# Kernel tuning notes

Hardware: AMD Instinct MI355X
Metric: run time of the kernel (lower is better)

The kernel has to match this reference:

```python
import jax, jax.numpy as jnp
import numpy as np

EPS = 1e-12


def setup_inputs() -> dict:
    key = jax.random.key(0)
    k1, k2, k3, k4, k5, k6 = jax.random.split(key, 6)
    N, R, T, D, depth = 50000, 1000, 400000, 256, 2
    features = jax.random.normal(k1, (N, D), dtype=jnp.float32)
    rel_emb = jax.random.normal(k2, (R, D), dtype=jnp.float32)
    # xavier-style scale for [D,1] kernels, stored as [depth, D]
    attn_kernels = jax.random.normal(k3, (depth, D), dtype=jnp.float32) * np.sqrt(2.0 / (D + 1))
    r_val = jnp.ones((T,), dtype=jnp.float32)
    adj = jax.random.randint(k4, (2, T), 0, N, dtype=jnp.int64)
    r_index_tri = jnp.arange(T, dtype=jnp.int64)  # one relation per triple
    r_index_rel = jax.random.randint(k5, (T,), 0, R, dtype=jnp.int64)
    return {
        "features": features,
        "rel_emb": rel_emb,
        "attn_kernels": attn_kernels,
        "r_val": r_val,
        "adj": adj,
        "r_index_tri": r_index_tri,
        "r_index_rel": r_index_rel,
    }


def reference(features, rel_emb, attn_kernels, r_val, adj, r_index_tri, r_index_rel):
    N, D = features.shape
    T = adj.shape[1]
    depth = attn_kernels.shape[0]
    dst, src = adj[0], adj[1]  # softmax/aggregate over dst rows, gather neighbors via src

    x = jnp.tanh(features)
    outputs = [x]
    for l in range(depth):
        # sparse [T,R] @ rel_emb -> per-triple relation embedding [T, D]
        tri_rel = jax.ops.segment_sum(r_val[:, None] * rel_emb[r_index_rel], r_index_tri, num_segments=T)
        # L2 normalize per edge (torch F.normalize, eps=1e-12)
        norm = jnp.sqrt(jnp.sum(tri_rel * tri_rel, axis=1, keepdims=True))
        tri_rel = tri_rel / jnp.maximum(norm, EPS)
        # gather neighbor features and reflect across relation hyperplane
        neighs = x[src]  # [T, D]
        neighs = neighs - 2.0 * jnp.sum(neighs * tri_rel, axis=1, keepdims=True) * tri_rel
        # per-edge attention logits, segment softmax over destination rows
        att = tri_rel @ attn_kernels[l]  # [T]
        seg_max = jax.ops.segment_max(att, dst, num_segments=N)  # [N]
        e = jnp.exp(att - seg_max[dst])
        seg_sum = jax.ops.segment_sum(e, dst, num_segments=N)
        w = e / seg_sum[dst]  # [T]
        # scatter-sum weighted neighbor messages
        new_features = jax.ops.segment_sum(neighs * w[:, None], dst, num_segments=N)
        x = jnp.tanh(new_features)
        outputs.append(x)
    return jnp.concatenate(outputs, axis=-1)  # [N, D*(depth+1)]
```

## Files before the change

### kernel.cpp

```cpp
#include <hip/hip_runtime.h>
#include <hip/hip_bf16.h>
#include <hip/hip_fp16.h>

static constexpr int kN = 50000;
static constexpr int kR = 1000;
static constexpr int kT = 400000;
static constexpr int kD = 256;
static constexpr int kOutD = 768;
static constexpr int kNB = (kN + 255) / 256;

static constexpr size_t kOffRel16 = 2219008;
static constexpr size_t kOffXb0   = 2752512;
static constexpr size_t kXbBytes  = (size_t)kN * kD * 2;
static constexpr size_t kOffXb1   = kOffXb0 + kXbBytes;
static constexpr size_t kWsFull   = kOffXb1 + kXbBytes;
static constexpr int kShRowC = 1536;
static constexpr int kShOffC = 1024;

#define EPS_NORM 1e-12f

__device__ __forceinline__ float bf2f(__hip_bfloat16 h) { return __bfloat162float(h); }

__device__ __forceinline__ float4 h4f(ushort4 u) {
  float4 f;
  f.x = __half2float(__ushort_as_half(u.x));
  f.y = __half2float(__ushort_as_half(u.y));
  f.z = __half2float(__ushort_as_half(u.z));
  f.w = __half2float(__ushort_as_half(u.w));
  return f;
}

__device__ __forceinline__ float loadF(const void* p, int i, int f32m) {
  return f32m ? ((const float*)p)[i] : bf2f(((const __hip_bfloat16*)p)[i]);
}
__device__ __forceinline__ int loadI(const void* p, int i, int i64m) {
  return i64m ? (int)(((const long long*)p)[i]) : ((const int*)p)[i];
}

__global__ void __launch_bounds__(256) detect_kernel(
    const void* __restrict__ feat, const void* __restrict__ adj,
    int* __restrict__ flags) {
  __shared__ int s_f32, s_i64;
  if (threadIdx.x == 0) { s_f32 = 0; s_i64 = 1; }
  __syncthreads();
  const __hip_bfloat16* fb = (const __hip_bfloat16*)feat;
  for (int i = threadIdx.x; i < 4096; i += 256) {
    const float v = bf2f(fb[i]);
    if (!(fabsf(v) <= 64.f)) atomicExch(&s_f32, 1);
  }
  const int* ai = (const int*)adj;
  for (int i = threadIdx.x; i < 2048; i += 256) {
    if (ai[2 * i + 1] != 0) atomicExch(&s_i64, 0);
  }
  __syncthreads();
  if (threadIdx.x == 0) { flags[0] = s_f32; flags[1] = s_i64; }
}

__global__ void __launch_bounds__(256) relnorm_kernel(
    const void* __restrict__ rel_emb, const void* __restrict__ attn_k,
    __half* __restrict__ rel16, float* __restrict__ attL,
    const int* __restrict__ flags) {
  const int f32m = flags[0];
  const int r = blockIdx.x;
  const int d = threadIdx.x;
  const float v  = loadF(rel_emb, r * kD + d, f32m);
  const float k0 = loadF(attn_k, d, f32m);
  const float k1 = loadF(attn_k, kD + d, f32m);
  float ss = v * v, d0 = v * k0, d1 = v * k1;
#pragma unroll
  for (int off = 32; off > 0; off >>= 1) {
    ss += __shfl_xor(ss, off);
    d0 += __shfl_xor(d0, off);
    d1 += __shfl_xor(d1, off);
  }
  __shared__ float s_ss[4], s_d0[4], s_d1[4];
  const int wave = threadIdx.x >> 6, lane = threadIdx.x & 63;
  if (lane == 0) { s_ss[wave] = ss; s_d0[wave] = d0; s_d1[wave] = d1; }
  __syncthreads();
  const float tss = s_ss[0] + s_ss[1] + s_ss[2] + s_ss[3];
  const float inv = 1.0f / fmaxf(sqrtf(tss), EPS_NORM);
  rel16[r * kD + d] = __float2half(v * inv);
  if (threadIdx.x == 0) {
    attL[r]      = (s_d0[0] + s_d0[1] + s_d0[2] + s_d0[3]) * inv;
    attL[kR + r] = (s_d1[0] + s_d1[1] + s_d1[2] + s_d1[3]) * inv;
  }
}

__global__ void __launch_bounds__(256) x0_kernel(
    const void* __restrict__ feat, float* __restrict__ out,
    __half* __restrict__ xb, int xbRow, int xbOff,
    const int* __restrict__ flags) {
  const int f32m = flags[0];
  const int i4 = (blockIdx.x * 256 + threadIdx.x) * 4;
  float v0, v1, v2, v3;
  if (f32m) {
    const float4 f = ((const float4*)feat)[i4 >> 2];
    v0 = f.x; v1 = f.y; v2 = f.z; v3 = f.w;
  } else {
    union { ushort4 u; __hip_bfloat16 h[4]; } xu;
    xu.u = ((const ushort4*)feat)[i4 >> 2];
    v0 = bf2f(xu.h[0]); v1 = bf2f(xu.h[1]); v2 = bf2f(xu.h[2]); v3 = bf2f(xu.h[3]);
  }
  const int n = i4 >> 8, d = i4 & 255;
  float4 o; o.x = tanhf(v0); o.y = tanhf(v1); o.z = tanhf(v2); o.w = tanhf(v3);
  *(float4*)(out + (size_t)n * kOutD + d) = o;
  ushort4 h;
  h.x = __half_as_ushort(__float2half(o.x));
  h.y = __half_as_ushort(__float2half(o.y));
  h.z = __half_as_ushort(__float2half(o.z));
  h.w = __half_as_ushort(__float2half(o.w));
  *(ushort4*)(xb + (size_t)n * xbRow + xbOff + d) = h;
}

__global__ void __launch_bounds__(256) count_kernel(
    const void* __restrict__ adj, int* __restrict__ counts,
    const int* __restrict__ flags) {
  const int t = blockIdx.x * 256 + threadIdx.x;
  if (t >= kT) return;
  atomicAdd(&counts[loadI(adj, t, flags[1])], 1);
}

__global__ void __launch_bounds__(256) psum_kernel(
    const int* __restrict__ counts, int* __restrict__ partials) {
  const int i = blockIdx.x * 256 + threadIdx.x;
  int v = (i < kN) ? counts[i] : 0;
#pragma unroll
  for (int off = 32; off > 0; off >>= 1) v += __shfl_xor(v, off);
  __shared__ int sw[4];
  const int lane = threadIdx.x & 63, wv = threadIdx.x >> 6;
  if (lane == 0) sw[wv] = v;
  __syncthreads();
  if (threadIdx.x == 0) partials[blockIdx.x] = sw[0] + sw[1] + sw[2] + sw[3];
}

__global__ void __launch_bounds__(256) pscan_kernel(int* __restrict__ partials) {
  const int tid = threadIdx.x, lane = tid & 63, wv = tid >> 6;
  const int v = (tid < kNB) ? partials[tid] : 0;
  int x = v;
#pragma unroll
  for (int d = 1; d < 64; d <<= 1) {
    const int y = __shfl_up(x, d);
    if (lane >= d) x += y;
  }
  __shared__ int sw[4];
  if (lane == 63) sw[wv] = x;
  __syncthreads();
  int woff = 0;
  for (int w = 0; w < wv; ++w) woff += sw[w];
  if (tid < kNB) partials[tid] = woff + x - v;
}

__global__ void __launch_bounds__(256) offs_kernel(
    const int* __restrict__ counts, const int* __restrict__ partials,
    int* __restrict__ offsets, int* __restrict__ cursor) {
  const int i = blockIdx.x * 256 + threadIdx.x;
  const int lane = threadIdx.x & 63, wv = threadIdx.x >> 6;
  const int v = (i < kN) ? counts[i] : 0;
  int x = v;
#pragma unroll
  for (int d = 1; d < 64; d <<= 1) {
    const int y = __shfl_up(x, d);
    if (lane >= d) x += y;
  }
  __shared__ int sw[4];
  if (lane == 63) sw[wv] = x;
  __syncthreads();
  int woff = 0;
  for (int w = 0; w < wv; ++w) woff += sw[w];
  const int excl = partials[blockIdx.x] + woff + x - v;
  if (i < kN) { offsets[i] = excl; cursor[i] = excl; }
  if (i == 0) offsets[kN] = kT;
}

__global__ void __launch_bounds__(256) fill_kernel(
    const void* __restrict__ adj, int* __restrict__ cursor,
    int* __restrict__ perm, const int* __restrict__ flags) {
  const int t = blockIdx.x * 256 + threadIdx.x;
  if (t >= kT) return;
  const int d = loadI(adj, t, flags[1]);
  perm[atomicAdd(&cursor[d], 1)] = t;
}

template <int XF16>
__global__ void __launch_bounds__(256, 6) layer_kernel(
    const void* __restrict__ adj, const void* __restrict__ rrel,
    const void* __restrict__ r_val,
    const int* __restrict__ offsets, const int* __restrict__ perm,
    const float* __restrict__ xin,
    const __half* __restrict__ xbin, int xbRow, int xbOff,
    const __half* __restrict__ rel16, const float* __restrict__ attL_l,
    float* __restrict__ out, int col0,
    __half* __restrict__ xbout,
    const int* __restrict__ flags) {
  const int f32m = flags[0], i64m = flags[1];
  const int lane = threadIdx.x & 63;
  const int n = blockIdx.x * 4 + (threadIdx.x >> 6);
  const int beg = offsets[n];
  const int cnt = offsets[n + 1] - beg;
  float4 acc = make_float4(0.f, 0.f, 0.f, 0.f);
  float* orow = out + (size_t)n * kOutD + col0;

  if (cnt > 0 && cnt <= 64) {
    int pk_l = 0;
    float logit = -1e30f;
    if (lane < cnt) {
      const int t = perm[beg + lane];
      const float rv = loadF(r_val, t, f32m);
      const int r  = loadI(rrel, t, i64m);
      const int sn = loadI(adj, kT + t, i64m);
      const float sgn = (rv > 0.f) ? 1.f : ((rv < 0.f) ? -1.f : 0.f);
      logit = sgn * attL_l[r];
      pk_l = ((rv != 0.f ? 1 : 0) << 30) | (r << 17) | sn;
    }
    float m = logit;
    for (int off = 1; off < cnt; off <<= 1) m = fmaxf(m, __shfl_xor(m, off));
    const float e = (lane < cnt) ? __expf(logit - m) : 0.f;
    float s = e;
    for (int off = 1; off < cnt; off <<= 1) s += __shfl_xor(s, off);
    const float w_me = (lane < cnt) ? e / s : 0.f;

    for (int base = 0; base < cnt; base += 8) {
      int pk[8]; float wk[8];
#pragma unroll
      for (int k = 0; k < 8; ++k) {
        pk[k] = __shfl(pk_l, base + k);
        wk[k] = __shfl(w_me, base + k);
      }
      ushort4 ux[8], ur[8]; float4 xf[8];
#pragma unroll
      for (int k = 0; k < 8; ++k) {
        const int sn = pk[k] & 0x1FFFF;
        const int r  = (pk[k] >> 17) & 0x1FFF;
        if (XF16) ux[k] = *(const ushort4*)(xbin + (size_t)sn * xbRow + xbOff + lane * 4);
        else      xf[k] = *(const float4*)(xin + (size_t)sn * kOutD + lane * 4);
        ur[k] = *(const ushort4*)(rel16 + ((size_t)r << 8) + lane * 4);
      }
      float4 rn[8]; float dt[8];
#pragma unroll
      for (int k = 0; k < 8; ++k) {
        const float4 xv = XF16 ? h4f(ux[k]) : xf[k];
        rn[k] = h4f(ur[k]);
        dt[k] = xv.x * rn[k].x + xv.y * rn[k].y + xv.z * rn[k].z + xv.w * rn[k].w;
        acc.x += xv.x * wk[k]; acc.y += xv.y * wk[k];
        acc.z += xv.z * wk[k]; acc.w += xv.w * wk[k];
      }
#pragma unroll
      for (int off = 32; off > 0; off >>= 1) {
#pragma unroll
        for (int k = 0; k < 8; ++k) dt[k] += __shfl_xor(dt[k], off);
      }
#pragma unroll
      for (int k = 0; k < 8; ++k) {
        const float c = (((pk[k] >> 30) & 1) ? 2.f * wk[k] : 0.f) * dt[k];
        acc.x -= c * rn[k].x; acc.y -= c * rn[k].y;
        acc.z -= c * rn[k].z; acc.w -= c * rn[k].w;
      }
    }
  } else if (cnt > 64) {
    float lm = -1e30f;
    for (int i = lane; i < cnt; i += 64) {
      const int t = perm[beg + i];
      const float rv = loadF(r_val, t, f32m);
      const float sgn = (rv > 0.f) ? 1.f : ((rv < 0.f) ? -1.f : 0.f);
      lm = fmaxf(lm, sgn * attL_l[loadI(rrel, t, i64m)]);
    }
#pragma unroll
    for (int off = 32; off > 0; off >>= 1) lm = fmaxf(lm, __shfl_xor(lm, off));
    float ls = 0.f;
    for (int i = lane; i < cnt; i += 64) {
      const int t = perm[beg + i];
      const float rv = loadF(r_val, t, f32m);
      const float sgn = (rv > 0.f) ? 1.f : ((rv < 0.f) ? -1.f : 0.f);
      ls += __expf(sgn * attL_l[loadI(rrel, t, i64m)] - lm);
    }
#pragma unroll
    for (int off = 32; off > 0; off >>= 1) ls += __shfl_xor(ls, off);
    const float inv_s = 1.f / ls;

    for (int base = 0; base < cnt; base += 64) {
      const int nIn = min(64, cnt - base);
      int sn_l = 0, r_l = 0;
      float w_l = 0.f, s2_l = 0.f;
      if (lane < nIn) {
        const int t = perm[beg + base + lane];
        const float rv = loadF(r_val, t, f32m);
        r_l  = loadI(rrel, t, i64m);
        sn_l = loadI(adj, kT + t, i64m);
        const float sgn = (rv > 0.f) ? 1.f : ((rv < 0.f) ? -1.f : 0.f);
        w_l = __expf(sgn * attL_l[r_l] - lm) * inv_s;
        s2_l = (rv != 0.f) ? 1.f : 0.f;
      }
      for (int k = 0; k < nIn; ++k) {
        const int sn   = __shfl(sn_l, k);
        const int r    = __shfl(r_l, k);
        const float w  = __shfl(w_l, k);
        const float s2 = __shfl(s2_l, k);
        float4 xv;
        if (XF16) {
          xv = h4f(*(const ushort4*)(xbin + (size_t)sn * xbRow + xbOff + lane * 4));
        } else {
          xv = *(const float4*)(xin + (size_t)sn * kOutD + lane * 4);
        }
        const float4 rn = h4f(*(const ushort4*)(rel16 + ((size_t)r << 8) + lane * 4));
        float dot = xv.x * rn.x + xv.y * rn.y + xv.z * rn.z + xv.w * rn.w;
#pragma unroll
        for (int off = 32; off > 0; off >>= 1) dot += __shfl_xor(dot, off);
        const float c = 2.f * s2 * dot * w;
        acc.x += xv.x * w - c * rn.x;
        acc.y += xv.y * w - c * rn.y;
        acc.z += xv.z * w - c * rn.z;
        acc.w += xv.w * w - c * rn.w;
      }
    }
  }

  acc.x = tanhf(acc.x); acc.y = tanhf(acc.y);
  acc.z = tanhf(acc.z); acc.w = tanhf(acc.w);
  *(float4*)(orow + lane * 4) = acc;
  if (XF16 && xbout) {
    ushort4 h;
    h.x = __half_as_ushort(__float2half(acc.x));
    h.y = __half_as_ushort(__float2half(acc.y));
    h.z = __half_as_ushort(__float2half(acc.z));
    h.w = __half_as_ushort(__float2half(acc.w));
    *(ushort4*)(xbout + (size_t)n * kD + lane * 4) = h;
  }
}

extern "C" void kernel_launch(void* const* d_in, const int* in_sizes, int n_in,
                              void* d_out, int out_size, void* d_ws, size_t ws_size,
                              hipStream_t stream) {
  const void* features = d_in[0];
  const void* rel_emb  = d_in[1];
  const void* attn_k   = d_in[2];
  const void* r_val    = d_in[3];
  const void* adj      = d_in[4];
  const void* rrel     = d_in[6];
  float* out           = (float*)d_out;

  char* ws = (char*)d_ws;
  int*    flags    = (int*)(ws + 0);
  float*  attL     = (float*)(ws + 4096);
  int*    partials = (int*)(ws + 12288);
  int*    counts   = (int*)(ws + 16384);
  int*    offsets  = (int*)(ws + 217088);
  int*    cursor   = (int*)(ws + 417792);
  int*    perm     = (int*)(ws + 618496);
  __half* rel16    = (__half*)(ws + kOffRel16);
  const bool full = (ws_size >= kWsFull);
  __half* xb0 = full ? (__half*)(ws + kOffXb0) : (__half*)out;
  __half* xb1 = full ? (__half*)(ws + kOffXb1) : nullptr;
  const int xbRow0 = full ? kD : kShRowC;
  const int xbOff0 = full ? 0  : kShOffC;

  const int tb = (kT + 255) / 256;

  detect_kernel<<<1, 256, 0, stream>>>(features, adj, flags);
  relnorm_kernel<<<kR, 256, 0, stream>>>(rel_emb, attn_k, rel16, attL, flags);
  x0_kernel<<<kN * kD / 1024, 256, 0, stream>>>(features, out, xb0, xbRow0,
                                                xbOff0, flags);

  hipMemsetAsync(counts, 0, (size_t)kN * 4, stream);
  count_kernel<<<tb, 256, 0, stream>>>(adj, counts, flags);
  psum_kernel<<<kNB, 256, 0, stream>>>(counts, partials);
  pscan_kernel<<<1, 256, 0, stream>>>(partials);
  offs_kernel<<<kNB, 256, 0, stream>>>(counts, partials, offsets, cursor);
  fill_kernel<<<tb, 256, 0, stream>>>(adj, cursor, perm, flags);

  layer_kernel<1><<<kN / 4, 256, 0, stream>>>(adj, rrel, r_val, offsets, perm,
                                              nullptr, xb0, xbRow0, xbOff0,
                                              rel16, attL, out, kD, xb1, flags);
  if (full) {
    layer_kernel<1><<<kN / 4, 256, 0, stream>>>(adj, rrel, r_val, offsets, perm,
                                                nullptr, xb1, kD, 0,
                                                rel16, attL + kR, out, 2 * kD,
                                                nullptr, flags);
  } else {
    layer_kernel<0><<<kN / 4, 256, 0, stream>>>(adj, rrel, r_val, offsets, perm,
                                                out + kD, nullptr, 0, 0,
                                                rel16, attL + kR, out, 2 * kD,
                                                nullptr, flags);
  }
}
```

Measured before the change: 425.8 us.

## Pack edge metadata in fill, software-pipeline gathers with scalar-base inline loads

```diff
diff --git a/kernel.cpp b/kernel.cpp
--- a/kernel.cpp
+++ b/kernel.cpp
@@ -10,24 +10,51 @@
 static constexpr int kNB = (kN + 255) / 256;
 
 static constexpr size_t kOffRel16 = 2219008;
-static constexpr size_t kOffXb0   = 2752512;
+static constexpr size_t kOffXb1   = 2752512;
 static constexpr size_t kXbBytes  = (size_t)kN * kD * 2;
-static constexpr size_t kOffXb1   = kOffXb0 + kXbBytes;
-static constexpr size_t kWsFull   = kOffXb1 + kXbBytes;
-static constexpr int kShRowC = 1536;
-static constexpr int kShOffC = 1024;
+static constexpr size_t kWsNeed   = kOffXb1 + kXbBytes;
+static constexpr int kShRowB = 3072;
+static constexpr int kShOffB = 2048;
 
 #define EPS_NORM 1e-12f
 
+typedef unsigned int u32;
+typedef unsigned long long u64;
+typedef u32 u32x2_t __attribute__((ext_vector_type(2)));
+typedef u32 u32x4_t __attribute__((ext_vector_type(4)));
+
 __device__ __forceinline__ float bf2f(__hip_bfloat16 h) { return __bfloat162float(h); }
 
-__device__ __forceinline__ float4 h4f(ushort4 u) {
+__device__ __forceinline__ float4 cvt8(u32x2_t u) {
   float4 f;
-  f.x = __half2float(__ushort_as_half(u.x));
-  f.y = __half2float(__ushort_as_half(u.y));
-  f.z = __half2float(__ushort_as_half(u.z));
-  f.w = __half2float(__ushort_as_half(u.w));
+  f.x = __half2float(__ushort_as_half((unsigned short)(u.x & 0xFFFFu)));
+  f.y = __half2float(__ushort_as_half((unsigned short)(u.x >> 16)));
+  f.z = __half2float(__ushort_as_half((unsigned short)(u.y & 0xFFFFu)));
+  f.w = __half2float(__ushort_as_half((unsigned short)(u.y >> 16)));
   return f;
+}
+__device__ __forceinline__ float4 asf4(u32x4_t u) {
+  float4 f;
+  f.x = __uint_as_float(u.x); f.y = __uint_as_float(u.y);
+  f.z = __uint_as_float(u.z); f.w = __uint_as_float(u.w);
+  return f;
+}
+
+__device__ __forceinline__ u32x2_t gload8(u64 sbase, u32 voff) {
+  u32x2_t r;
+  asm volatile("global_load_dwordx2 %0, %1, %2"
+               : "=v"(r) : "v"(voff), "s"(sbase) : "memory");
+  return r;
+}
+__device__ __forceinline__ u32x4_t gload16(u64 sbase, u32 voff) {
+  u32x4_t r;
+  asm volatile("global_load_dwordx4 %0, %1, %2"
+               : "=v"(r) : "v"(voff), "s"(sbase) : "memory");
+  return r;
+}
+__device__ __forceinline__ void waitv0() {
+  asm volatile("s_waitcnt vmcnt(0)" ::: "memory");
+  __builtin_amdgcn_sched_barrier(0);
 }
 
 __device__ __forceinline__ float loadF(const void* p, int i, int f32m) {
@@ -88,7 +115,6 @@
 
 __global__ void __launch_bounds__(256) x0_kernel(
     const void* __restrict__ feat, float* __restrict__ out,
-    __half* __restrict__ xb, int xbRow, int xbOff,
     const int* __restrict__ flags) {
   const int f32m = flags[0];
   const int i4 = (blockIdx.x * 256 + threadIdx.x) * 4;
@@ -109,7 +135,7 @@
   h.y = __half_as_ushort(__float2half(o.y));
   h.z = __half_as_ushort(__float2half(o.z));
   h.w = __half_as_ushort(__float2half(o.w));
-  *(ushort4*)(xb + (size_t)n * xbRow + xbOff + d) = h;
+  *(ushort4*)((char*)out + (size_t)n * kShRowB + kShOffB + (size_t)d * 2) = h;
 }
 
 __global__ void __launch_bounds__(256) count_kernel(
@@ -173,26 +199,29 @@
 }
 
 __global__ void __launch_bounds__(256) fill_kernel(
-    const void* __restrict__ adj, int* __restrict__ cursor,
+    const void* __restrict__ adj, const void* __restrict__ rrel,
+    const void* __restrict__ r_val, int* __restrict__ cursor,
     int* __restrict__ perm, const int* __restrict__ flags) {
   const int t = blockIdx.x * 256 + threadIdx.x;
   if (t >= kT) return;
-  const int d = loadI(adj, t, flags[1]);
-  perm[atomicAdd(&cursor[d], 1)] = t;
-}
-
-template <int XF16>
-__global__ void __launch_bounds__(256, 6) layer_kernel(
-    const void* __restrict__ adj, const void* __restrict__ rrel,
-    const void* __restrict__ r_val,
+  const int f32m = flags[0], i64m = flags[1];
+  const int dn = loadI(adj, t, i64m);
+  const int sn = loadI(adj, kT + t, i64m);
+  const int r  = loadI(rrel, t, i64m);
+  const float rv = loadF(r_val, t, f32m);
+  const int pk = (sn & 0xFFFF) | ((r & 0x3FF) << 16) |
+                 ((rv != 0.f) ? (1 << 26) : 0) | ((rv < 0.f) ? (1 << 27) : 0);
+  perm[atomicAdd(&cursor[dn], 1)] = pk;
+}
+
+template <int XF16, int XROWB, int XOFFB>
+__global__ void __launch_bounds__(256, 5) layer_kernel(
     const int* __restrict__ offsets, const int* __restrict__ perm,
     const float* __restrict__ xin,
-    const __half* __restrict__ xbin, int xbRow, int xbOff,
+    const char* __restrict__ xb,
     const __half* __restrict__ rel16, const float* __restrict__ attL_l,
     float* __restrict__ out, int col0,
-    __half* __restrict__ xbout,
-    const int* __restrict__ flags) {
-  const int f32m = flags[0], i64m = flags[1];
+    __half* __restrict__ xbout) {
   const int lane = threadIdx.x & 63;
   const int n = blockIdx.x * 4 + (threadIdx.x >> 6);
   const int beg = offsets[n];
@@ -204,14 +233,59 @@
     int pk_l = 0;
     float logit = -1e30f;
     if (lane < cnt) {
-      const int t = perm[beg + lane];
-      const float rv = loadF(r_val, t, f32m);
-      const int r  = loadI(rrel, t, i64m);
-      const int sn = loadI(adj, kT + t, i64m);
-      const float sgn = (rv > 0.f) ? 1.f : ((rv < 0.f) ? -1.f : 0.f);
-      logit = sgn * attL_l[r];
-      pk_l = ((rv != 0.f ? 1 : 0) << 30) | (r << 17) | sn;
+      pk_l = perm[beg + lane];
+      const float a = attL_l[(pk_l >> 16) & 0x3FF];
+      const float sa = (pk_l & (1 << 27)) ? -a : a;
+      logit = (pk_l & (1 << 26)) ? sa : 0.f;
     }
+    asm volatile("" : "+v"(logit));
+
+    const u32 voffx = (u32)lane * (XF16 ? 8u : 16u);
+    const u32 voffr = (u32)lane * 8u;
+    u32x2_t ux2[8]; u32x4_t ux4[8]; u32x2_t ur[8];
+
+#define ISSUE_BATCH(BASE)                                                      \
+  _Pragma("unroll") for (int k = 0; k < 8; ++k) {                              \
+    const u32 p = (u32)__builtin_amdgcn_readlane(pk_l, (BASE) + k);            \
+    if (XF16) {                                                                \
+      ux2[k] = gload8((u64)xb + (u64)((p & 0xFFFFu) * (u32)XROWB) + (u32)XOFFB,\
+                      voffx);                                                  \
+    } else {                                                                   \
+      ux4[k] = gload16((u64)xin + (u64)((p & 0xFFFFu) * 3072u) + 1024u, voffx);\
+    }                                                                          \
+    ur[k] = gload8((u64)rel16 + (u64)(((p >> 16) & 0x3FFu) << 9), voffr);      \
+  }
+
+#define COMPUTE_BATCH(BASE)                                                    \
+  {                                                                            \
+    float dt[8];                                                               \
+    _Pragma("unroll") for (int k = 0; k < 8; ++k) {                            \
+      const float sw = __uint_as_float(                                        \
+          (u32)__builtin_amdgcn_readlane(__float_as_uint(w_me), (BASE) + k));  \
+      float4 xv;                                                               \
+      if (XF16) xv = cvt8(ux2[k]); else xv = asf4(ux4[k]);                     \
+      const float4 rr = cvt8(ur[k]);                                           \
+      dt[k] = xv.x * rr.x + xv.y * rr.y + xv.z * rr.z + xv.w * rr.w;           \
+      acc.x += xv.x * sw; acc.y += xv.y * sw;                                  \
+      acc.z += xv.z * sw; acc.w += xv.w * sw;                                  \
+    }                                                                          \
+    _Pragma("unroll") for (int off = 32; off > 0; off >>= 1) {                 \
+      _Pragma("unroll") for (int k = 0; k < 8; ++k)                            \
+        dt[k] += __shfl_xor(dt[k], off);                                       \
+    }                                                                          \
+    _Pragma("unroll") for (int k = 0; k < 8; ++k) {                            \
+      const u32 p = (u32)__builtin_amdgcn_readlane(pk_l, (BASE) + k);          \
+      const float sw = __uint_as_float(                                        \
+          (u32)__builtin_amdgcn_readlane(__float_as_uint(w_me), (BASE) + k));  \
+      const float cw = ((p >> 26) & 1u) ? (2.f * sw * dt[k]) : 0.f;            \
+      const float4 rr = cvt8(ur[k]);                                           \
+      acc.x -= cw * rr.x; acc.y -= cw * rr.y;                                  \
+      acc.z -= cw * rr.z; acc.w -= cw * rr.w;                                  \
+    }                                                                          \
+  }
+
+    ISSUE_BATCH(0);
+
     float m = logit;
     for (int off = 1; off < cnt; off <<= 1) m = fmaxf(m, __shfl_xor(m, off));
     const float e = (lane < cnt) ? __expf(logit - m) : 0.f;
@@ -219,59 +293,32 @@
     for (int off = 1; off < cnt; off <<= 1) s += __shfl_xor(s, off);
     const float w_me = (lane < cnt) ? e / s : 0.f;
 
-    for (int base = 0; base < cnt; base += 8) {
-      int pk[8]; float wk[8];
-#pragma unroll
-      for (int k = 0; k < 8; ++k) {
-        pk[k] = __shfl(pk_l, base + k);
-        wk[k] = __shfl(w_me, base + k);
-      }
-      ushort4 ux[8], ur[8]; float4 xf[8];
-#pragma unroll
-      for (int k = 0; k < 8; ++k) {
-        const int sn = pk[k] & 0x1FFFF;
-        const int r  = (pk[k] >> 17) & 0x1FFF;
-        if (XF16) ux[k] = *(const ushort4*)(xbin + (size_t)sn * xbRow + xbOff + lane * 4);
-        else      xf[k] = *(const float4*)(xin + (size_t)sn * kOutD + lane * 4);
-        ur[k] = *(const ushort4*)(rel16 + ((size_t)r << 8) + lane * 4);
-      }
-      float4 rn[8]; float dt[8];
-#pragma unroll
-      for (int k = 0; k < 8; ++k) {
-        const float4 xv = XF16 ? h4f(ux[k]) : xf[k];
-        rn[k] = h4f(ur[k]);
-        dt[k] = xv.x * rn[k].x + xv.y * rn[k].y + xv.z * rn[k].z + xv.w * rn[k].w;
-        acc.x += xv.x * wk[k]; acc.y += xv.y * wk[k];
-        acc.z += xv.z * wk[k]; acc.w += xv.w * wk[k];
-      }
-#pragma unroll
-      for (int off = 32; off > 0; off >>= 1) {
-#pragma unroll
-        for (int k = 0; k < 8; ++k) dt[k] += __shfl_xor(dt[k], off);
-      }
-#pragma unroll
-      for (int k = 0; k < 8; ++k) {
-        const float c = (((pk[k] >> 30) & 1) ? 2.f * wk[k] : 0.f) * dt[k];
-        acc.x -= c * rn[k].x; acc.y -= c * rn[k].y;
-        acc.z -= c * rn[k].z; acc.w -= c * rn[k].w;
-      }
+    int base = 0;
+    while (true) {
+      waitv0();
+      COMPUTE_BATCH(base);
+      base += 8;
+      if (base >= cnt) break;
+      ISSUE_BATCH(base);
     }
+#undef ISSUE_BATCH
+#undef COMPUTE_BATCH
   } else if (cnt > 64) {
     float lm = -1e30f;
     for (int i = lane; i < cnt; i += 64) {
-      const int t = perm[beg + i];
-      const float rv = loadF(r_val, t, f32m);
-      const float sgn = (rv > 0.f) ? 1.f : ((rv < 0.f) ? -1.f : 0.f);
-      lm = fmaxf(lm, sgn * attL_l[loadI(rrel, t, i64m)]);
+      const int p = perm[beg + i];
+      const float a = attL_l[(p >> 16) & 0x3FF];
+      const float sa = (p & (1 << 27)) ? -a : a;
+      lm = fmaxf(lm, (p & (1 << 26)) ? sa : 0.f);
     }
 #pragma unroll
     for (int off = 32; off > 0; off >>= 1) lm = fmaxf(lm, __shfl_xor(lm, off));
     float ls = 0.f;
     for (int i = lane; i < cnt; i += 64) {
-      const int t = perm[beg + i];
-      const float rv = loadF(r_val, t, f32m);
-      const float sgn = (rv > 0.f) ? 1.f : ((rv < 0.f) ? -1.f : 0.f);
-      ls += __expf(sgn * attL_l[loadI(rrel, t, i64m)] - lm);
+      const int p = perm[beg + i];
+      const float a = attL_l[(p >> 16) & 0x3FF];
+      const float sa = (p & (1 << 27)) ? -a : a;
+      ls += __expf(((p & (1 << 26)) ? sa : 0.f) - lm);
     }
 #pragma unroll
     for (int off = 32; off > 0; off >>= 1) ls += __shfl_xor(ls, off);
@@ -279,37 +326,36 @@
 
     for (int base = 0; base < cnt; base += 64) {
       const int nIn = min(64, cnt - base);
-      int sn_l = 0, r_l = 0;
-      float w_l = 0.f, s2_l = 0.f;
+      int pkl = 0; float wl = 0.f;
       if (lane < nIn) {
-        const int t = perm[beg + base + lane];
-        const float rv = loadF(r_val, t, f32m);
-        r_l  = loadI(rrel, t, i64m);
-        sn_l = loadI(adj, kT + t, i64m);
-        const float sgn = (rv > 0.f) ? 1.f : ((rv < 0.f) ? -1.f : 0.f);
-        w_l = __expf(sgn * attL_l[r_l] - lm) * inv_s;
-        s2_l = (rv != 0.f) ? 1.f : 0.f;
+        pkl = perm[beg + base + lane];
+        const float a = attL_l[(pkl >> 16) & 0x3FF];
+        const float sa = (pkl & (1 << 27)) ? -a : a;
+        wl = __expf(((pkl & (1 << 26)) ? sa : 0.f) - lm) * inv_s;
       }
       for (int k = 0; k < nIn; ++k) {
-        const int sn   = __shfl(sn_l, k);
-        const int r    = __shfl(r_l, k);
-        const float w  = __shfl(w_l, k);
-        const float s2 = __shfl(s2_l, k);
+        const int p   = __shfl(pkl, k);
+        const float w = __shfl(wl, k);
         float4 xv;
         if (XF16) {
-          xv = h4f(*(const ushort4*)(xbin + (size_t)sn * xbRow + xbOff + lane * 4));
+          xv = cvt8(*(const u32x2_t*)(xb + (size_t)(p & 0xFFFF) * XROWB +
+                                      XOFFB + (size_t)lane * 8));
         } else {
-          xv = *(const float4*)(xin + (size_t)sn * kOutD + lane * 4);
+          xv = *(const float4*)((const char*)xin + (size_t)(p & 0xFFFF) * 3072 +
+                                1024 + (size_t)lane * 16);
         }
-        const float4 rn = h4f(*(const ushort4*)(rel16 + ((size_t)r << 8) + lane * 4));
-        float dot = xv.x * rn.x + xv.y * rn.y + xv.z * rn.z + xv.w * rn.w;
+        const float4 rr = cvt8(*(const u32x2_t*)((const char*)rel16 +
+                               (((size_t)(p >> 16) & 0x3FF) << 9) +
+                               (size_t)lane * 8));
+        float dot = xv.x * rr.x + xv.y * rr.y + xv.z * rr.z + xv.w * rr.w;
 #pragma unroll
         for (int off = 32; off > 0; off >>= 1) dot += __shfl_xor(dot, off);
+        const float s2 = (p >> 26) & 1 ? 1.f : 0.f;
         const float c = 2.f * s2 * dot * w;
-        acc.x += xv.x * w - c * rn.x;
-        acc.y += xv.y * w - c * rn.y;
-        acc.z += xv.z * w - c * rn.z;
-        acc.w += xv.w * w - c * rn.w;
+        acc.x += xv.x * w - c * rr.x;
+        acc.y += xv.y * w - c * rr.y;
+        acc.z += xv.z * w - c * rr.z;
+        acc.w += xv.w * w - c * rr.w;
       }
     }
   }
@@ -317,7 +363,7 @@
   acc.x = tanhf(acc.x); acc.y = tanhf(acc.y);
   acc.z = tanhf(acc.z); acc.w = tanhf(acc.w);
   *(float4*)(orow + lane * 4) = acc;
-  if (XF16 && xbout) {
+  if (xbout) {
     ushort4 h;
     h.x = __half_as_ushort(__float2half(acc.x));
     h.y = __half_as_ushort(__float2half(acc.y));
@@ -347,38 +393,30 @@
   int*    cursor   = (int*)(ws + 417792);
   int*    perm     = (int*)(ws + 618496);
   __half* rel16    = (__half*)(ws + kOffRel16);
-  const bool full = (ws_size >= kWsFull);
-  __half* xb0 = full ? (__half*)(ws + kOffXb0) : (__half*)out;
+  const bool full = (ws_size >= kWsNeed);
   __half* xb1 = full ? (__half*)(ws + kOffXb1) : nullptr;
-  const int xbRow0 = full ? kD : kShRowC;
-  const int xbOff0 = full ? 0  : kShOffC;
 
   const int tb = (kT + 255) / 256;
 
   detect_kernel<<<1, 256, 0, stream>>>(features, adj, flags);
   relnorm_kernel<<<kR, 256, 0, stream>>>(rel_emb, attn_k, rel16, attL, flags);
-  x0_kernel<<<kN * kD / 1024, 256, 0, stream>>>(features, out, xb0, xbRow0,
-                                                xbOff0, flags);
+  x0_kernel<<<kN * kD / 1024, 256, 0, stream>>>(features, out, flags);
 
   hipMemsetAsync(counts, 0, (size_t)kN * 4, stream);
   count_kernel<<<tb, 256, 0, stream>>>(adj, counts, flags);
   psum_kernel<<<kNB, 256, 0, stream>>>(counts, partials);
   pscan_kernel<<<1, 256, 0, stream>>>(partials);
   offs_kernel<<<kNB, 256, 0, stream>>>(counts, partials, offsets, cursor);
-  fill_kernel<<<tb, 256, 0, stream>>>(adj, cursor, perm, flags);
-
-  layer_kernel<1><<<kN / 4, 256, 0, stream>>>(adj, rrel, r_val, offsets, perm,
-                                              nullptr, xb0, xbRow0, xbOff0,
-                                              rel16, attL, out, kD, xb1, flags);
+  fill_kernel<<<tb, 256, 0, stream>>>(adj, rrel, r_val, cursor, perm, flags);
+
+  layer_kernel<1, kShRowB, kShOffB><<<kN / 4, 256, 0, stream>>>(
+      offsets, perm, nullptr, (const char*)out, rel16, attL, out, kD, xb1);
   if (full) {
-    layer_kernel<1><<<kN / 4, 256, 0, stream>>>(adj, rrel, r_val, offsets, perm,
-                                                nullptr, xb1, kD, 0,
-                                                rel16, attL + kR, out, 2 * kD,
-                                                nullptr, flags);
+    layer_kernel<1, 512, 0><<<kN / 4, 256, 0, stream>>>(
+        offsets, perm, nullptr, (const char*)xb1, rel16, attL + kR, out,
+        2 * kD, nullptr);
   } else {
-    layer_kernel<0><<<kN / 4, 256, 0, stream>>>(adj, rrel, r_val, offsets, perm,
-                                                out + kD, nullptr, 0, 0,
-                                                rel16, attL + kR, out, 2 * kD,
-                                                nullptr, flags);
-  }
-}
+    layer_kernel<0, 1, 0><<<kN / 4, 256, 0, stream>>>(
+        offsets, perm, out, nullptr, rel16, attL + kR, out, 2 * kD, nullptr);
+  }
+}
```

After: 389.2 us. 1.09x faster.
